# Optimization experiments

Hardware: AMD Instinct MI355X
Metric: run time of the kernel (lower is better)

Reference implementation:

```python
import jax, jax.numpy as jnp
import numpy as np

KV_H, Q_H, ATT_H = 256, 256, 128
B, S, SQ = 2, 1024, 512

def setup_inputs() -> dict:
    key = jax.random.key(0)
    ks = jax.random.split(key, 8)
    sc = lambda d: 1.0 / np.sqrt(d)
    return {
        "attention_kv": jax.random.normal(ks[0], (B, S, KV_H), dtype=jnp.float32),
        "attention_query": jax.random.normal(ks[1], (B, SQ, Q_H), dtype=jnp.float32),
        "W_kv": jax.random.uniform(ks[2], (KV_H, ATT_H), jnp.float32, -sc(KV_H), sc(KV_H)),
        "b_kv": jax.random.uniform(ks[3], (ATT_H,), jnp.float32, -sc(KV_H), sc(KV_H)),
        "W_q": jax.random.uniform(ks[4], (Q_H, ATT_H), jnp.float32, -sc(Q_H), sc(Q_H)),
        "b_q": jax.random.uniform(ks[5], (ATT_H,), jnp.float32, -sc(Q_H), sc(Q_H)),
        "w_v": jax.random.uniform(ks[6], (ATT_H,), jnp.float32, -sc(ATT_H), sc(ATT_H)),
        "b_v": jax.random.uniform(ks[7], (), jnp.float32, -sc(ATT_H), sc(ATT_H)),
    }

def reference(attention_kv, attention_query, W_kv, b_kv, W_q, b_q, w_v, b_v):
    # proj_kv: (B, S, A); proj_q: (B, Sq, A)
    proj_kv = jnp.einsum('bsh,ha->bsa', attention_kv, W_kv) + b_kv
    proj_q = jnp.einsum('bqh,ha->bqa', attention_query, W_q) + b_q
    # broadcast add + tanh -> (B, Sq, S, A)
    hidden = jnp.tanh(proj_kv[:, None, :, :] + proj_q[:, :, None, :])
    # scalar score per (b, q, s)
    attention_score = jnp.einsum('bqsa,a->bqs', hidden, w_v) + b_v
    attention_weight = jax.nn.softmax(attention_score, axis=-1)
    # weighted sum over kv sequence -> (B, Sq, KV_H)
    attention_output = jnp.einsum('bqs,bsh->bqh', attention_weight, attention_kv)
    return attention_output, attention_weight
```

## Files before the change

kernel.cpp:

```cpp
#include <hip/hip_runtime.h>
#include <hip/hip_bf16.h>

#define NB   2
#define SKV  1024
#define NSQ  512
#define HIN  256
#define HA   128

#define KSC   2.8853900817779268f
#define LOG2E 1.4426950408889634f

__global__ __launch_bounds__(128) void proj_kernel(
    const float* __restrict__ kv,
    const float* __restrict__ qy,
    const float* __restrict__ Wkv,
    const float* __restrict__ bkv,
    const float* __restrict__ Wq,
    const float* __restrict__ bq,
    float* __restrict__ ek,
    float* __restrict__ eq)
{
    const int t  = threadIdx.x;
    const int r0 = blockIdx.x * 8;
    const bool is_q = (r0 >= NB * SKV);
    const float* __restrict__ src = is_q ? (qy + (size_t)(r0 - NB * SKV) * HIN)
                                         : (kv + (size_t)r0 * HIN);
    const float* __restrict__ W  = is_q ? Wq : Wkv;
    const float* __restrict__ bs = is_q ? bq : bkv;
    float* __restrict__ dst = is_q ? (eq + (size_t)(r0 - NB * SKV) * HA)
                                   : (ek + (size_t)r0 * HA);

    float a[8];
    #pragma unroll
    for (int i = 0; i < 8; ++i) a[i] = 0.f;

    #pragma unroll 2
    for (int h = 0; h < HIN; h += 4) {
        float w0 = W[(h + 0) * HA + t];
        float w1 = W[(h + 1) * HA + t];
        float w2 = W[(h + 2) * HA + t];
        float w3 = W[(h + 3) * HA + t];
        #pragma unroll
        for (int i = 0; i < 8; ++i) {
            const float4 r = *(const float4*)(src + (size_t)i * HIN + h);
            a[i] = fmaf(r.x, w0, a[i]);
            a[i] = fmaf(r.y, w1, a[i]);
            a[i] = fmaf(r.z, w2, a[i]);
            a[i] = fmaf(r.w, w3, a[i]);
        }
    }
    const float bb = bs[t];
    #pragma unroll
    for (int i = 0; i < 8; ++i)
        dst[(size_t)i * HA + t] = __builtin_amdgcn_exp2f((a[i] + bb) * KSC);
}

__global__ __launch_bounds__(512) void attn_kernel(
    const float* __restrict__ ek,
    const float* __restrict__ eq,
    const float* __restrict__ wv,
    const float* __restrict__ bv,
    const float* __restrict__ kv,
    float* __restrict__ out)
{
    __shared__ __align__(16) float eq_s[4][HA];
    __shared__ __align__(16) float wv_s[HA];
    __shared__ __align__(16) float wt_s[SKV][4];
    __shared__ float red[2][4][8];
    __shared__ float w0red[8];
    __shared__ __align__(16) float part[8][4][HIN];

    const int tid  = threadIdx.x;
    const int lane = tid & 63, wid = tid >> 6;
    const int bq0  = blockIdx.x * 4;
    const int b    = bq0 >> 9;

    {
        const int row = tid >> 7, a = tid & 127;
        eq_s[row][a] = eq[(size_t)(bq0 + row) * HA + a];
    }
    float w0p = (tid < HA) ? wv[tid] : 0.f;
    if (tid < HA) wv_s[tid] = w0p;
    #pragma unroll
    for (int o = 32; o > 0; o >>= 1) w0p += __shfl_down(w0p, o);
    if (lane == 0) w0red[wid] = w0p;
    const float bvf = bv[0];
    __syncthreads();
    float W0 = 0.f;
    #pragma unroll
    for (int i = 0; i < 8; ++i) W0 += w0red[i];

    float acc[4][2];
    #pragma unroll
    for (int q = 0; q < 4; ++q) { acc[q][0] = 0.f; acc[q][1] = 0.f; }
    {
        const float4* __restrict__ e0row = (const float4*)(ek + (size_t)(b * SKV + tid) * HA);
        const float4* __restrict__ e1row = (const float4*)(ek + (size_t)(b * SKV + tid + 512) * HA);
        const float4* __restrict__ wv4 = (const float4*)wv_s;
        const float4* __restrict__ q40 = (const float4*)&eq_s[0][0];
        const float4* __restrict__ q41 = (const float4*)&eq_s[1][0];
        const float4* __restrict__ q42 = (const float4*)&eq_s[2][0];
        const float4* __restrict__ q43 = (const float4*)&eq_s[3][0];
        #pragma unroll 2
        for (int a4 = 0; a4 < 32; ++a4) {
            const float4 E0 = e0row[a4];
            const float4 E1 = e1row[a4];
            const float4 w4 = wv4[a4];
            float4 qq[4];
            qq[0] = q40[a4]; qq[1] = q41[a4]; qq[2] = q42[a4]; qq[3] = q43[a4];
            const float* Ep0 = (const float*)&E0;
            const float* Ep1 = (const float*)&E1;
            const float* Wp  = (const float*)&w4;
            #pragma unroll
            for (int c = 0; c < 4; ++c) {
                const float e0c = Ep0[c], e1c = Ep1[c], wc = Wp[c];
                #pragma unroll
                for (int q = 0; q < 4; ++q) {
                    const float qc = ((const float*)&qq[q])[c];
                    const float x  = fmaf(e0c, qc, 1.f);
                    const float y  = fmaf(e1c, qc, 1.f);
                    const float r  = __builtin_amdgcn_rcpf(x * y);
                    acc[q][0] = fmaf(wc, r * y, acc[q][0]);
                    acc[q][1] = fmaf(wc, r * x, acc[q][1]);
                }
            }
        }
    }
    float sc[4][2];
    #pragma unroll
    for (int q = 0; q < 4; ++q) {
        sc[q][0] = fmaf(-2.f, acc[q][0], W0) + bvf;
        sc[q][1] = fmaf(-2.f, acc[q][1], W0) + bvf;
    }

    #pragma unroll
    for (int q = 0; q < 4; ++q) {
        float m = fmaxf(sc[q][0], sc[q][1]);
        #pragma unroll
        for (int o = 32; o > 0; o >>= 1) m = fmaxf(m, __shfl_down(m, o));
        if (lane == 0) red[0][q][wid] = m;
    }
    __syncthreads();
    float M[4];
    #pragma unroll
    for (int q = 0; q < 4; ++q) {
        float m = red[0][q][0];
        #pragma unroll
        for (int i = 1; i < 8; ++i) m = fmaxf(m, red[0][q][i]);
        M[q] = m;
    }
    float e[4][2];
    #pragma unroll
    for (int q = 0; q < 4; ++q) {
        e[q][0] = __builtin_amdgcn_exp2f((sc[q][0] - M[q]) * LOG2E);
        e[q][1] = __builtin_amdgcn_exp2f((sc[q][1] - M[q]) * LOG2E);
        float sum = e[q][0] + e[q][1];
        #pragma unroll
        for (int o = 32; o > 0; o >>= 1) sum += __shfl_down(sum, o);
        if (lane == 0) red[1][q][wid] = sum;
    }
    __syncthreads();
    float rw[4];
    #pragma unroll
    for (int q = 0; q < 4; ++q) {
        float d = red[1][q][0];
        #pragma unroll
        for (int i = 1; i < 8; ++i) d += red[1][q][i];
        rw[q] = 1.0f / d;
    }

    float* __restrict__ outw = out + (size_t)NB * NSQ * HIN;
    #pragma unroll
    for (int si = 0; si < 2; ++si) {
        const int s = si * 512 + tid;
        #pragma unroll
        for (int q = 0; q < 4; ++q) {
            const float w = e[q][si] * rw[q];
            wt_s[s][q] = w;
            outw[(size_t)(bq0 + q) * SKV + s] = w;
        }
    }
    __syncthreads();

    {
        const int g = wid;
        float4 ac0 = {0,0,0,0}, ac1 = {0,0,0,0}, ac2 = {0,0,0,0}, ac3 = {0,0,0,0};
        const float4* __restrict__ kvb =
            (const float4*)(kv + (size_t)(b * SKV + g * 128) * HIN);
        #pragma unroll 4
        for (int i = 0; i < 128; ++i) {
            const int s = g * 128 + i;
            const float4 w4 = *((const float4*)&wt_s[s][0]);
            const float4 v  = kvb[(size_t)i * 64 + lane];
            ac0.x = fmaf(w4.x, v.x, ac0.x); ac0.y = fmaf(w4.x, v.y, ac0.y);
            ac0.z = fmaf(w4.x, v.z, ac0.z); ac0.w = fmaf(w4.x, v.w, ac0.w);
            ac1.x = fmaf(w4.y, v.x, ac1.x); ac1.y = fmaf(w4.y, v.y, ac1.y);
            ac1.z = fmaf(w4.y, v.z, ac1.z); ac1.w = fmaf(w4.y, v.w, ac1.w);
            ac2.x = fmaf(w4.z, v.x, ac2.x); ac2.y = fmaf(w4.z, v.y, ac2.y);
            ac2.z = fmaf(w4.z, v.z, ac2.z); ac2.w = fmaf(w4.z, v.w, ac2.w);
            ac3.x = fmaf(w4.w, v.x, ac3.x); ac3.y = fmaf(w4.w, v.y, ac3.y);
            ac3.z = fmaf(w4.w, v.z, ac3.z); ac3.w = fmaf(w4.w, v.w, ac3.w);
        }
        ((float4*)part[g][0])[lane] = ac0;
        ((float4*)part[g][1])[lane] = ac1;
        ((float4*)part[g][2])[lane] = ac2;
        ((float4*)part[g][3])[lane] = ac3;
    }
    __syncthreads();
    #pragma unroll
    for (int k = 0; k < 2; ++k) {
        const int id = tid + k * 512;
        const int q = id >> 8, h = id & 255;
        float v = 0.f;
        #pragma unroll
        for (int g2 = 0; g2 < 8; ++g2) v += part[g2][q][h];
        out[(size_t)(bq0 + q) * HIN + h] = v;
    }
}

extern "C" void kernel_launch(void* const* d_in, const int* in_sizes, int n_in,
                              void* d_out, int out_size, void* d_ws, size_t ws_size,
                              hipStream_t stream) {
    (void)in_sizes; (void)n_in; (void)out_size; (void)ws_size;
    const float* kv  = (const float*)d_in[0];
    const float* qy  = (const float*)d_in[1];
    const float* Wkv = (const float*)d_in[2];
    const float* bkv = (const float*)d_in[3];
    const float* Wq  = (const float*)d_in[4];
    const float* bq  = (const float*)d_in[5];
    const float* wv  = (const float*)d_in[6];
    const float* bv  = (const float*)d_in[7];

    float* ek = (float*)d_ws;
    float* eq = ek + (size_t)NB * SKV * HA;
    float* out = (float*)d_out;

    hipLaunchKernelGGL(proj_kernel, dim3((NB * SKV + NB * NSQ) / 8), dim3(128), 0, stream,
                       kv, qy, Wkv, bkv, Wq, bq, ek, eq);
    hipLaunchKernelGGL(attn_kernel, dim3(NB * NSQ / 4), dim3(512), 0, stream,
                       ek, eq, wv, bv, kv, out);
}
```

Baseline: 128.3 us.

## Split attention into score and output kernels with packed FMA math

Replaces the fused attention kernel with two kernels. A score kernel handles 8 queries per block over half the KV sequence and writes unnormalized exp scores plus partial denominators. An output kernel normalizes the scores and does the weighted KV sum over half the hidden dimension per block. The projection kernel and both new kernels also switch to packed v2f FMAs and wider vector loads. Softmax max-subtraction is dropped, which relies on scores staying bounded, and the score matrix now makes an extra round trip through global memory.

Result: faster. 124.6 us (-2.9%).

```diff
diff --git a/kernel.cpp b/kernel.cpp
--- a/kernel.cpp
+++ b/kernel.cpp
@@ -10,7 +10,12 @@
 #define KSC   2.8853900817779268f
 #define LOG2E 1.4426950408889634f
 
-__global__ __launch_bounds__(128) void proj_kernel(
+typedef float v2f __attribute__((ext_vector_type(2)));
+__device__ __forceinline__ v2f pkfma(v2f a, v2f b, v2f c) {
+    return __builtin_elementwise_fma(a, b, c);
+}
+
+__global__ __launch_bounds__(256) void proj_kernel(
     const float* __restrict__ kv,
     const float* __restrict__ qy,
     const float* __restrict__ Wkv,
@@ -21,6 +26,8 @@
     float* __restrict__ eq)
 {
     const int t  = threadIdx.x;
+    const int c4 = (t & 31) * 4;
+    const int r  = t >> 5;
     const int r0 = blockIdx.x * 8;
     const bool is_q = (r0 >= NB * SKV);
     const float* __restrict__ src = is_q ? (qy + (size_t)(r0 - NB * SKV) * HIN)
@@ -30,191 +37,217 @@
     float* __restrict__ dst = is_q ? (eq + (size_t)(r0 - NB * SKV) * HA)
                                    : (ek + (size_t)r0 * HA);
 
-    float a[8];
-    #pragma unroll
-    for (int i = 0; i < 8; ++i) a[i] = 0.f;
-
-    #pragma unroll 2
-    for (int h = 0; h < HIN; h += 4) {
-        float w0 = W[(h + 0) * HA + t];
-        float w1 = W[(h + 1) * HA + t];
-        float w2 = W[(h + 2) * HA + t];
-        float w3 = W[(h + 3) * HA + t];
-        #pragma unroll
-        for (int i = 0; i < 8; ++i) {
-            const float4 r = *(const float4*)(src + (size_t)i * HIN + h);
-            a[i] = fmaf(r.x, w0, a[i]);
-            a[i] = fmaf(r.y, w1, a[i]);
-            a[i] = fmaf(r.z, w2, a[i]);
-            a[i] = fmaf(r.w, w3, a[i]);
-        }
-    }
-    const float bb = bs[t];
-    #pragma unroll
-    for (int i = 0; i < 8; ++i)
-        dst[(size_t)i * HA + t] = __builtin_amdgcn_exp2f((a[i] + bb) * KSC);
-}
-
-__global__ __launch_bounds__(512) void attn_kernel(
+    const float* __restrict__ row = src + (size_t)r * HIN;
+    v2f a0 = {0.f, 0.f}, a1 = {0.f, 0.f};
+    #pragma unroll 4
+    for (int h4 = 0; h4 < 64; ++h4) {
+        const float4 x = *(const float4*)(row + h4 * 4);
+        const float* Wb = W + (size_t)h4 * 4 * HA + c4;
+        const float4 w0 = *(const float4*)(Wb);
+        const float4 w1 = *(const float4*)(Wb + HA);
+        const float4 w2 = *(const float4*)(Wb + 2 * HA);
+        const float4 w3 = *(const float4*)(Wb + 3 * HA);
+        a0 = pkfma((v2f){w0.x, w0.y}, (v2f){x.x, x.x}, a0);
+        a1 = pkfma((v2f){w0.z, w0.w}, (v2f){x.x, x.x}, a1);
+        a0 = pkfma((v2f){w1.x, w1.y}, (v2f){x.y, x.y}, a0);
+        a1 = pkfma((v2f){w1.z, w1.w}, (v2f){x.y, x.y}, a1);
+        a0 = pkfma((v2f){w2.x, w2.y}, (v2f){x.z, x.z}, a0);
+        a1 = pkfma((v2f){w2.z, w2.w}, (v2f){x.z, x.z}, a1);
+        a0 = pkfma((v2f){w3.x, w3.y}, (v2f){x.w, x.w}, a0);
+        a1 = pkfma((v2f){w3.z, w3.w}, (v2f){x.w, x.w}, a1);
+    }
+    const float4 bb = *(const float4*)(bs + c4);
+    float4 o;
+    o.x = __builtin_amdgcn_exp2f((a0.x + bb.x) * KSC);
+    o.y = __builtin_amdgcn_exp2f((a0.y + bb.y) * KSC);
+    o.z = __builtin_amdgcn_exp2f((a1.x + bb.z) * KSC);
+    o.w = __builtin_amdgcn_exp2f((a1.y + bb.w) * KSC);
+    *(float4*)(dst + (size_t)r * HA + c4) = o;
+}
+
+__global__ __launch_bounds__(512) void score_kernel(
     const float* __restrict__ ek,
     const float* __restrict__ eq,
     const float* __restrict__ wv,
     const float* __restrict__ bv,
+    float* __restrict__ ew,
+    float* __restrict__ Dp)
+{
+    __shared__ __align__(16) float4 eqs[8][32];
+    __shared__ __align__(16) float4 wvs[32];
+    __shared__ float w0red[8];
+    __shared__ float dred[8][8];
+
+    const int t    = threadIdx.x;
+    const int lane = t & 63, wid = t >> 6;
+    const int blk  = blockIdx.x;
+    const int sh   = blk & 1;
+    const int oct  = blk >> 1;
+    const int q0   = oct * 8;
+    const int b    = q0 >> 9;
+    const int s    = sh * 512 + t;
+
+    if (t < 256) {
+        const int j = t >> 5, f = t & 31;
+        eqs[j][f] = *((const float4*)(eq + (size_t)(q0 + j) * HA) + f);
+    } else if (t < 288) {
+        wvs[t - 256] = ((const float4*)wv)[t - 256];
+    }
+    float w0p = wv[t & 127];
+    #pragma unroll
+    for (int o = 32; o > 0; o >>= 1) w0p += __shfl_down(w0p, o);
+    if (lane == 0) w0red[wid] = w0p;
+    const float bvf = bv[0];
+    __syncthreads();
+    const float W0 = w0red[0] + w0red[1];
+
+    const float4* __restrict__ Erow4 = (const float4*)(ek + (size_t)(b * SKV + s) * HA);
+    v2f acc[8];
+    #pragma unroll
+    for (int j = 0; j < 8; ++j) acc[j] = (v2f){0.f, 0.f};
+    const v2f one = {1.f, 1.f};
+    #pragma unroll 2
+    for (int a4 = 0; a4 < 32; ++a4) {
+        const float4 E  = Erow4[a4];
+        const float4 w4 = wvs[a4];
+        const v2f E01 = {E.x, E.y};
+        const v2f E23 = {E.z, E.w};
+        const v2f w01 = {w4.x, w4.y};
+        const v2f w23 = {w4.z, w4.w};
+        #pragma unroll
+        for (int j = 0; j < 8; ++j) {
+            const float4 qv = eqs[j][a4];
+            const v2f A  = pkfma(E01, (v2f){qv.x, qv.y}, one);
+            const v2f B  = pkfma(E23, (v2f){qv.z, qv.w}, one);
+            const v2f m  = A * B;
+            const float r = __builtin_amdgcn_rcpf(m.x * m.y);
+            const v2f ts = (v2f){m.y, m.x} * (v2f){r, r};
+            acc[j] = pkfma(w01, ts * B, acc[j]);
+            acc[j] = pkfma(w23, ts * A, acc[j]);
+        }
+    }
+
+    float ev[8];
+    #pragma unroll
+    for (int j = 0; j < 8; ++j) {
+        const float score = fmaf(-2.f, acc[j].x + acc[j].y, W0) + bvf;
+        ev[j] = __builtin_amdgcn_exp2f(score * LOG2E);
+        ew[(size_t)(q0 + j) * SKV + s] = ev[j];
+    }
+    #pragma unroll
+    for (int j = 0; j < 8; ++j) {
+        float ss = ev[j];
+        #pragma unroll
+        for (int o = 32; o > 0; o >>= 1) ss += __shfl_down(ss, o);
+        if (lane == 0) dred[wid][j] = ss;
+    }
+    __syncthreads();
+    if (t < 8) {
+        float d = 0.f;
+        #pragma unroll
+        for (int w = 0; w < 8; ++w) d += dred[w][t];
+        Dp[(size_t)sh * 1024 + q0 + t] = d;
+    }
+}
+
+__global__ __launch_bounds__(512) void out_kernel(
+    const float* __restrict__ ew,
+    const float* __restrict__ Dp,
     const float* __restrict__ kv,
     float* __restrict__ out)
 {
-    __shared__ __align__(16) float eq_s[4][HA];
-    __shared__ __align__(16) float wv_s[HA];
-    __shared__ __align__(16) float wt_s[SKV][4];
-    __shared__ float red[2][4][8];
-    __shared__ float w0red[8];
-    __shared__ __align__(16) float part[8][4][HIN];
-
-    const int tid  = threadIdx.x;
-    const int lane = tid & 63, wid = tid >> 6;
-    const int bq0  = blockIdx.x * 4;
-    const int b    = bq0 >> 9;
-
-    {
-        const int row = tid >> 7, a = tid & 127;
-        eq_s[row][a] = eq[(size_t)(bq0 + row) * HA + a];
-    }
-    float w0p = (tid < HA) ? wv[tid] : 0.f;
-    if (tid < HA) wv_s[tid] = w0p;
-    #pragma unroll
-    for (int o = 32; o > 0; o >>= 1) w0p += __shfl_down(w0p, o);
-    if (lane == 0) w0red[wid] = w0p;
-    const float bvf = bv[0];
-    __syncthreads();
-    float W0 = 0.f;
-    #pragma unroll
-    for (int i = 0; i < 8; ++i) W0 += w0red[i];
-
-    float acc[4][2];
-    #pragma unroll
-    for (int q = 0; q < 4; ++q) { acc[q][0] = 0.f; acc[q][1] = 0.f; }
-    {
-        const float4* __restrict__ e0row = (const float4*)(ek + (size_t)(b * SKV + tid) * HA);
-        const float4* __restrict__ e1row = (const float4*)(ek + (size_t)(b * SKV + tid + 512) * HA);
-        const float4* __restrict__ wv4 = (const float4*)wv_s;
-        const float4* __restrict__ q40 = (const float4*)&eq_s[0][0];
-        const float4* __restrict__ q41 = (const float4*)&eq_s[1][0];
-        const float4* __restrict__ q42 = (const float4*)&eq_s[2][0];
-        const float4* __restrict__ q43 = (const float4*)&eq_s[3][0];
-        #pragma unroll 2
-        for (int a4 = 0; a4 < 32; ++a4) {
-            const float4 E0 = e0row[a4];
-            const float4 E1 = e1row[a4];
-            const float4 w4 = wv4[a4];
-            float4 qq[4];
-            qq[0] = q40[a4]; qq[1] = q41[a4]; qq[2] = q42[a4]; qq[3] = q43[a4];
-            const float* Ep0 = (const float*)&E0;
-            const float* Ep1 = (const float*)&E1;
-            const float* Wp  = (const float*)&w4;
+    __shared__ __align__(16) float lds[SKV * 12];
+    __shared__ float rws[8];
+
+    const int t    = threadIdx.x;
+    const int lane = t & 63, wid = t >> 6;
+    const int blk  = blockIdx.x;
+    const int hh   = blk & 1;
+    const int oct  = blk >> 1;
+    const int q0   = oct * 8;
+    const int b    = q0 >> 9;
+
+    if (t < 8) rws[t] = 1.0f / (Dp[q0 + t] + Dp[1024 + q0 + t]);
+    __syncthreads();
+    float rw[8];
+    #pragma unroll
+    for (int j = 0; j < 8; ++j) rw[j] = rws[j];
+
+    float* __restrict__ outw = out + (size_t)NB * NSQ * HIN;
+    #pragma unroll
+    for (int p = 0; p < 2; ++p) {
+        const int s = wid * 128 + p * 64 + lane;
+        float e[8];
+        #pragma unroll
+        for (int j = 0; j < 8; ++j) e[j] = ew[(size_t)(q0 + j) * SKV + s] * rw[j];
+        if (hh == 0) {
             #pragma unroll
-            for (int c = 0; c < 4; ++c) {
-                const float e0c = Ep0[c], e1c = Ep1[c], wc = Wp[c];
-                #pragma unroll
-                for (int q = 0; q < 4; ++q) {
-                    const float qc = ((const float*)&qq[q])[c];
-                    const float x  = fmaf(e0c, qc, 1.f);
-                    const float y  = fmaf(e1c, qc, 1.f);
-                    const float r  = __builtin_amdgcn_rcpf(x * y);
-                    acc[q][0] = fmaf(wc, r * y, acc[q][0]);
-                    acc[q][1] = fmaf(wc, r * x, acc[q][1]);
-                }
-            }
+            for (int j = 0; j < 8; ++j) outw[(size_t)(q0 + j) * SKV + s] = e[j];
         }
-    }
-    float sc[4][2];
-    #pragma unroll
-    for (int q = 0; q < 4; ++q) {
-        sc[q][0] = fmaf(-2.f, acc[q][0], W0) + bvf;
-        sc[q][1] = fmaf(-2.f, acc[q][1], W0) + bvf;
-    }
-
-    #pragma unroll
-    for (int q = 0; q < 4; ++q) {
-        float m = fmaxf(sc[q][0], sc[q][1]);
-        #pragma unroll
-        for (int o = 32; o > 0; o >>= 1) m = fmaxf(m, __shfl_down(m, o));
-        if (lane == 0) red[0][q][wid] = m;
-    }
-    __syncthreads();
-    float M[4];
-    #pragma unroll
-    for (int q = 0; q < 4; ++q) {
-        float m = red[0][q][0];
-        #pragma unroll
-        for (int i = 1; i < 8; ++i) m = fmaxf(m, red[0][q][i]);
-        M[q] = m;
-    }
-    float e[4][2];
-    #pragma unroll
-    for (int q = 0; q < 4; ++q) {
-        e[q][0] = __builtin_amdgcn_exp2f((sc[q][0] - M[q]) * LOG2E);
-        e[q][1] = __builtin_amdgcn_exp2f((sc[q][1] - M[q]) * LOG2E);
-        float sum = e[q][0] + e[q][1];
-        #pragma unroll
-        for (int o = 32; o > 0; o >>= 1) sum += __shfl_down(sum, o);
-        if (lane == 0) red[1][q][wid] = sum;
-    }
-    __syncthreads();
-    float rw[4];
-    #pragma unroll
-    for (int q = 0; q < 4; ++q) {
-        float d = red[1][q][0];
-        #pragma unroll
-        for (int i = 1; i < 8; ++i) d += red[1][q][i];
-        rw[q] = 1.0f / d;
-    }
-
-    float* __restrict__ outw = out + (size_t)NB * NSQ * HIN;
-    #pragma unroll
-    for (int si = 0; si < 2; ++si) {
-        const int s = si * 512 + tid;
-        #pragma unroll
-        for (int q = 0; q < 4; ++q) {
-            const float w = e[q][si] * rw[q];
-            wt_s[s][q] = w;
-            outw[(size_t)(bq0 + q) * SKV + s] = w;
+        float* d = lds + (size_t)s * 12;
+        *(float4*)(d)     = make_float4(e[0], e[1], e[2], e[3]);
+        *(float4*)(d + 4) = make_float4(e[4], e[5], e[6], e[7]);
+    }
+    __syncthreads();
+
+    const int hq  = t & 31;
+    const int sc0 = t >> 5;
+    const int h   = hh * 128 + hq * 4;
+    const float* __restrict__ kvb = kv + (size_t)b * SKV * HIN + h;
+    v2f acc[8][2];
+    #pragma unroll
+    for (int j = 0; j < 8; ++j) { acc[j][0] = (v2f){0.f, 0.f}; acc[j][1] = (v2f){0.f, 0.f}; }
+    #pragma unroll 4
+    for (int i = 0; i < 64; ++i) {
+        const int s = sc0 * 64 + i;
+        const float4 v = *(const float4*)(kvb + (size_t)s * HIN);
+        const float* er = lds + (size_t)s * 12;
+        const float4 e03 = *(const float4*)(er);
+        const float4 e47 = *(const float4*)(er + 4);
+        const v2f vlo = {v.x, v.y}, vhi = {v.z, v.w};
+        acc[0][0] = pkfma(vlo, (v2f){e03.x, e03.x}, acc[0][0]);
+        acc[0][1] = pkfma(vhi, (v2f){e03.x, e03.x}, acc[0][1]);
+        acc[1][0] = pkfma(vlo, (v2f){e03.y, e03.y}, acc[1][0]);
+        acc[1][1] = pkfma(vhi, (v2f){e03.y, e03.y}, acc[1][1]);
+        acc[2][0] = pkfma(vlo, (v2f){e03.z, e03.z}, acc[2][0]);
+        acc[2][1] = pkfma(vhi, (v2f){e03.z, e03.z}, acc[2][1]);
+        acc[3][0] = pkfma(vlo, (v2f){e03.w, e03.w}, acc[3][0]);
+        acc[3][1] = pkfma(vhi, (v2f){e03.w, e03.w}, acc[3][1]);
+        acc[4][0] = pkfma(vlo, (v2f){e47.x, e47.x}, acc[4][0]);
+        acc[4][1] = pkfma(vhi, (v2f){e47.x, e47.x}, acc[4][1]);
+        acc[5][0] = pkfma(vlo, (v2f){e47.y, e47.y}, acc[5][0]);
+        acc[5][1] = pkfma(vhi, (v2f){e47.y, e47.y}, acc[5][1]);
+        acc[6][0] = pkfma(vlo, (v2f){e47.z, e47.z}, acc[6][0]);
+        acc[6][1] = pkfma(vhi, (v2f){e47.z, e47.z}, acc[6][1]);
+        acc[7][0] = pkfma(vlo, (v2f){e47.w, e47.w}, acc[7][0]);
+        acc[7][1] = pkfma(vhi, (v2f){e47.w, e47.w}, acc[7][1]);
+    }
+
+    #pragma unroll
+    for (int j = 0; j < 8; ++j) {
+        #pragma unroll
+        for (int k = 0; k < 2; ++k) {
+            acc[j][k].x += __shfl_down(acc[j][k].x, 32);
+            acc[j][k].y += __shfl_down(acc[j][k].y, 32);
         }
     }
     __syncthreads();
-
-    {
-        const int g = wid;
-        float4 ac0 = {0,0,0,0}, ac1 = {0,0,0,0}, ac2 = {0,0,0,0}, ac3 = {0,0,0,0};
-        const float4* __restrict__ kvb =
-            (const float4*)(kv + (size_t)(b * SKV + g * 128) * HIN);
-        #pragma unroll 4
-        for (int i = 0; i < 128; ++i) {
-            const int s = g * 128 + i;
-            const float4 w4 = *((const float4*)&wt_s[s][0]);
-            const float4 v  = kvb[(size_t)i * 64 + lane];
-            ac0.x = fmaf(w4.x, v.x, ac0.x); ac0.y = fmaf(w4.x, v.y, ac0.y);
-            ac0.z = fmaf(w4.x, v.z, ac0.z); ac0.w = fmaf(w4.x, v.w, ac0.w);
-            ac1.x = fmaf(w4.y, v.x, ac1.x); ac1.y = fmaf(w4.y, v.y, ac1.y);
-            ac1.z = fmaf(w4.y, v.z, ac1.z); ac1.w = fmaf(w4.y, v.w, ac1.w);
-            ac2.x = fmaf(w4.z, v.x, ac2.x); ac2.y = fmaf(w4.z, v.y, ac2.y);
-            ac2.z = fmaf(w4.z, v.z, ac2.z); ac2.w = fmaf(w4.z, v.w, ac2.w);
-            ac3.x = fmaf(w4.w, v.x, ac3.x); ac3.y = fmaf(w4.w, v.y, ac3.y);
-            ac3.z = fmaf(w4.w, v.z, ac3.z); ac3.w = fmaf(w4.w, v.w, ac3.w);
-        }
-        ((float4*)part[g][0])[lane] = ac0;
-        ((float4*)part[g][1])[lane] = ac1;
-        ((float4*)part[g][2])[lane] = ac2;
-        ((float4*)part[g][3])[lane] = ac3;
+    if (lane < 32) {
+        float* pp = lds + (size_t)wid * 1024 + hq * 4;
+        #pragma unroll
+        for (int j = 0; j < 8; ++j)
+            *(float4*)(pp + (size_t)j * 128) =
+                make_float4(acc[j][0].x, acc[j][0].y, acc[j][1].x, acc[j][1].y);
     }
     __syncthreads();
     #pragma unroll
     for (int k = 0; k < 2; ++k) {
-        const int id = tid + k * 512;
-        const int q = id >> 8, h = id & 255;
+        const int id = t + k * 512;
+        const int j = id >> 7, hl = id & 127;
         float v = 0.f;
         #pragma unroll
-        for (int g2 = 0; g2 < 8; ++g2) v += part[g2][q][h];
-        out[(size_t)(bq0 + q) * HIN + h] = v;
+        for (int g = 0; g < 8; ++g) v += lds[(size_t)g * 1024 + j * 128 + hl];
+        out[(size_t)(q0 + j) * HIN + hh * 128 + hl] = v;
     }
 }
 
@@ -232,11 +265,15 @@
     const float* bv  = (const float*)d_in[7];
 
     float* ek = (float*)d_ws;
-    float* eq = ek + (size_t)NB * SKV * HA;
+    float* eq = ek + 262144;
+    float* ew = eq + 131072;
+    float* Dp = ew + 1048576;
     float* out = (float*)d_out;
 
-    hipLaunchKernelGGL(proj_kernel, dim3((NB * SKV + NB * NSQ) / 8), dim3(128), 0, stream,
+    hipLaunchKernelGGL(proj_kernel, dim3(384), dim3(256), 0, stream,
                        kv, qy, Wkv, bkv, Wq, bq, ek, eq);
-    hipLaunchKernelGGL(attn_kernel, dim3(NB * NSQ / 4), dim3(512), 0, stream,
-                       ek, eq, wv, bv, kv, out);
-}
+    hipLaunchKernelGGL(score_kernel, dim3(256), dim3(512), 0, stream,
+                       ek, eq, wv, bv, ew, Dp);
+    hipLaunchKernelGGL(out_kernel, dim3(256), dim3(512), 0, stream,
+                       ew, Dp, kv, out);
+}
```
